# Optimization experiments

Hardware: AMD Instinct MI355X
Metric: run time of the kernel (lower is better)

## Reference

```python
import jax, jax.numpy as jnp
import numpy as np
import math

STRIDES = [4, 8, 16, 32, 64]
SCALES  = [32, 64, 128, 256, 512]
RATIOS  = [2.0, 1.0, 0.5]
GRIDS   = [(200, 304), (100, 152), (50, 76), (25, 38), (13, 19)]  # 800x1216 canvas
LSZ     = [gh * gw * 3 for gh, gw in GRIDS]                        # anchors per level
PRE_NMS_K = [min(1000, n) for n in LSZ]                            # select_by_score (1000, lsz)
IMG_H, IMG_W = 800, 1216
BBOX_CLAMP = math.log(1000.0 / 16.0)
IOU_TH = 0.7
MAX_OUT = 1000
MIN_SIZE = 1e-2
LEVEL_OFFSET = 1e4  # batched-NMS level separation offset


def _make_priors():
    # post.get_priors with loc='corner': anchor centers at stride*i (no +0.5)
    out = []
    for st, (gh, gw), sc in zip(STRIDES, GRIDS, SCALES):
        anc = []
        for r in RATIOS:  # make_anchors_rounded: 1 scale x 3 ratios, rounded
            h = sc * np.sqrt(r)
            w = sc / np.sqrt(r)
            anc.append(np.round(np.array([-w / 2, -h / 2, w / 2, h / 2])))
        anc = np.stack(anc)  # [3,4]
        ys = (np.arange(gh) * st).astype(np.float32)
        xs = (np.arange(gw) * st).astype(np.float32)
        yy, xx = np.meshgrid(ys, xs, indexing='ij')
        shifts = np.stack([xx, yy, xx, yy], axis=-1).reshape(-1, 1, 4)  # [gh*gw,1,4]
        out.append((shifts + anc[None].astype(np.float32)).reshape(-1, 4))
    return np.concatenate(out).astype(np.float32)  # [A,4]


def setup_inputs() -> dict:
    key = jax.random.key(0)
    k1, k2 = jax.random.split(key)
    B, A = 16, sum(LSZ)
    reg = jax.random.normal(k1, (B, A, 4), dtype=jnp.float32) * 0.5  # box deltas
    obj = jax.random.normal(k2, (B, A, 1), dtype=jnp.float32)        # objectness logits
    priors = jnp.asarray(_make_priors())
    return {"reg": reg, "obj": obj, "priors": priors}


def _nms(boxes, init_keep):
    # sequential NMS over score-sorted boxes; boxes already level-offset. [N,4]
    N = boxes.shape[0]
    areas = jnp.clip(boxes[:, 2] - boxes[:, 0], 0) * jnp.clip(boxes[:, 3] - boxes[:, 1], 0)
    rng = jnp.arange(N)

    def body(i, keep):
        b = boxes[i]
        xx1 = jnp.maximum(b[0], boxes[:, 0])
        yy1 = jnp.maximum(b[1], boxes[:, 1])
        xx2 = jnp.minimum(b[2], boxes[:, 2])
        yy2 = jnp.minimum(b[3], boxes[:, 3])
        inter = jnp.clip(xx2 - xx1, 0) * jnp.clip(yy2 - yy1, 0)
        iou = inter / (areas[i] + areas - inter + 1e-9)
        sup = (iou > IOU_TH) & (rng > i) & keep[i]
        return keep & ~sup

    return jax.lax.fori_loop(0, N, body, init_keep)


def reference(reg, obj, priors):
    B = reg.shape[0]
    scores = jax.nn.sigmoid(obj[..., 0])  # [B,A]

    # per-level top-k selection (select_by_score with (1000, lsz))
    off = 0
    idxs, scs, levs = [], [], []
    for l, (n, k) in enumerate(zip(LSZ, PRE_NMS_K)):
        sv, si = jax.lax.top_k(scores[:, off:off + n], k)
        idxs.append(si + off)
        scs.append(sv)
        levs.append(np.full(k, l, np.int32))
        off += n
    idx = jnp.concatenate(idxs, axis=1)       # [B,N] global anchor indices
    sc = jnp.concatenate(scs, axis=1)         # [B,N]
    levels = jnp.asarray(np.concatenate(levs))  # [N]

    reg_s = jnp.take_along_axis(reg, idx[..., None], axis=1)  # [B,N,4]
    pri_s = priors[idx]                                        # [B,N,4]

    # decode_boxes, settings=(1, 1, log(1000/16))
    pw = pri_s[..., 2] - pri_s[..., 0]
    ph = pri_s[..., 3] - pri_s[..., 1]
    pcx = pri_s[..., 0] + 0.5 * pw
    pcy = pri_s[..., 1] + 0.5 * ph
    dx, dy = reg_s[..., 0], reg_s[..., 1]
    dw = jnp.minimum(reg_s[..., 2], BBOX_CLAMP)
    dh = jnp.minimum(reg_s[..., 3], BBOX_CLAMP)
    cx = dx * pw + pcx
    cy = dy * ph + pcy
    w = pw * jnp.exp(dw)
    h = ph * jnp.exp(dh)
    boxes = jnp.stack([cx - 0.5 * w, cy - 0.5 * h, cx + 0.5 * w, cy + 0.5 * h], axis=-1)

    # clamp_to_canvas
    boxes = jnp.stack([
        jnp.clip(boxes[..., 0], 0, IMG_W), jnp.clip(boxes[..., 1], 0, IMG_H),
        jnp.clip(boxes[..., 2], 0, IMG_W), jnp.clip(boxes[..., 3], 0, IMG_H)], axis=-1)

    # remove_small
    small_ok = ((boxes[..., 2] - boxes[..., 0]) > MIN_SIZE) & ((boxes[..., 3] - boxes[..., 1]) > MIN_SIZE)

    # global score-descending order for NMS
    order = jnp.argsort(-sc, axis=1)
    boxes = jnp.take_along_axis(boxes, order[..., None], axis=1)
    sc = jnp.take_along_axis(sc, order, axis=1)
    small_ok = jnp.take_along_axis(small_ok, order, axis=1)
    lev = jnp.take_along_axis(jnp.broadcast_to(levels, sc.shape), order, axis=1)

    # per-level batched NMS via coordinate offset; NMS decisions are non-differentiable
    boxes_off = jax.lax.stop_gradient(boxes) + lev[..., None].astype(boxes.dtype) * LEVEL_OFFSET
    keep = jax.vmap(_nms)(boxes_off, small_ok)  # [B,N] bool

    # take first MAX_OUT kept (already score-sorted), pad with zeros
    rank = jnp.cumsum(keep, axis=1) - 1
    pos = jnp.where(keep & (rank < MAX_OUT), rank, MAX_OUT)  # dump slot MAX_OUT
    out_b = jax.vmap(lambda p, b: jnp.zeros((MAX_OUT + 1, 4), b.dtype).at[p].set(b))(pos, boxes)[:, :MAX_OUT]
    out_s = jax.vmap(lambda p, s: jnp.zeros((MAX_OUT + 1,), s.dtype).at[p].set(s))(pos, sc)[:, :MAX_OUT]
    return jnp.concatenate([out_b, out_s[..., None]], axis=-1)  # [B,1000,5]
```

## Files before the change

### kernel.cpp

```cpp
#include <hip/hip_runtime.h>

typedef unsigned int u32;
typedef unsigned short u16;
typedef unsigned long long u64;

#define NB 16
#define NA 242991
#define NSEL 4741

__device__ __constant__ int c_LN[5]   = {182400, 45600, 11400, 2850, 741};
__device__ __constant__ int c_LOFF[5] = {0, 182400, 228000, 239400, 242250};
__device__ __constant__ int c_LK[5]   = {1000, 1000, 1000, 1000, 741};
__device__ __constant__ int c_SOFF[5] = {0, 1000, 2000, 3000, 4000};
__device__ __constant__ int c_CST[5]  = {0, 64, 80, 84, 85};
__device__ __constant__ int c_CCN[5]  = {64, 16, 4, 1, 1};


__device__ __forceinline__ float xla_tanhf(float x) {
#pragma clang fp contract(off)
  float t = fminf(fmaxf(x, -9.0f), 9.0f);
  float x2 = t * t;
  float p = -2.76076847742355e-16f;
  p = p * x2 + 2.00018790482477e-13f;
  p = p * x2 + -8.60467152213735e-11f;
  p = p * x2 + 5.12229709037114e-08f;
  p = p * x2 + 1.48572235717979e-05f;
  p = p * x2 + 6.37261928875436e-04f;
  p = p * x2 + 4.89352455891786e-03f;
  p = t * p;
  float q = 1.19825839466702e-06f;
  q = q * x2 + 1.18534705686654e-04f;
  q = q * x2 + 2.26843463243900e-03f;
  q = q * x2 + 4.89352518554385e-03f;
  float r = p / q;
  return (fabsf(x) < 0.0004f) ? x : r;
}

__device__ __forceinline__ float ref_sigmoid(float x) {
#pragma clang fp contract(off)
  float t = 0.5f * x;
  float th = xla_tanhf(t);
  return 0.5f + 0.5f * th;
}

__device__ __forceinline__ float xla_expf(float x) {
#pragma clang fp contract(off)
  float fx = x * 1.44269504088896341f + 0.5f;
  fx = floorf(fx);
  float tmp = fx * 0.693359375f;
  float z = fx * -2.12194440e-4f;
  float r = x - tmp;
  r = r - z;
  float r2 = r * r;
  float y = 1.9875691500e-4f;
  y = y * r + 1.3981999507e-3f;
  y = y * r + 8.3334519073e-3f;
  y = y * r + 4.1665795894e-2f;
  y = y * r + 1.6666665459e-1f;
  y = y * r + 5.0000001201e-1f;
  y = y * r2 + r;
  y = y + 1.0f;
  int k = (int)fx;
  float two_k = __uint_as_float((u32)((k + 127) << 23));
  return y * two_k;
}

__device__ __forceinline__ void chunk_map(int c, int& l, int& base, int& n) {
  if (c < 64)      { l = 0; base = c * 2850;                 n = 2850; }
  else if (c < 80) { l = 1; base = 182400 + (c - 64) * 2850; n = 2850; }
  else if (c < 84) { l = 2; base = 228000 + (c - 80) * 2850; n = 2850; }
  else if (c == 84){ l = 3; base = 239400;                   n = 2850; }
  else             { l = 4; base = 242250;                   n = 741;  }
}


__global__ void __launch_bounds__(256) k_hist(const float* __restrict__ obj,
                                              u16* __restrict__ ghist) {
  const int c = blockIdx.x, b = blockIdx.y;
  int l, base, n;
  chunk_map(c, l, base, n);
  __shared__ u32 h[4096];
  for (int i = threadIdx.x; i < 4096; i += 256) h[i] = 0;
  __syncthreads();
  const float* src = obj + (size_t)b * NA + base;
  for (int i = threadIdx.x; i < n; i += 256) {
    float s = ref_sigmoid(src[i]);
    atomicAdd(&h[__float_as_uint(s) >> 18], 1u);
  }
  __syncthreads();
  u32* gh = (u32*)(ghist + ((size_t)b * 86 + c) * 4096);
  for (int i = threadIdx.x; i < 2048; i += 256)
    gh[i] = (h[2 * i] & 0xFFFFu) | (h[2 * i + 1] << 16);
}


__global__ void __launch_bounds__(1024) k_thresh(const u16* __restrict__ ghist,
                                                 int2* __restrict__ binfo,
                                                 u32* __restrict__ ctrs) {
  const int l = blockIdx.x, b = blockIdx.y, t = threadIdx.x;
  const int K = c_LK[l];
  const int bl = b * 5 + l;
  if (t == 0) { ctrs[bl] = 0; ctrs[80 + bl] = 0; }
  __shared__ u32 scan[1024];
  __shared__ int sh_b;
  __shared__ u32 sh_G;
  u32 h0 = 0, h1 = 0, h2 = 0, h3 = 0;
  const int cs = c_CST[l], cn = c_CCN[l];
  const u16* base = ghist + (size_t)b * 86 * 4096 + 4 * t;
  for (int cc = 0; cc < cn; ++cc) {
    uint2 v = *(const uint2*)(base + (size_t)(cs + cc) * 4096);
    h0 += v.x & 0xFFFFu; h1 += v.x >> 16;
    h2 += v.y & 0xFFFFu; h3 += v.y >> 16;
  }
  u32 loc = h0 + h1 + h2 + h3;
  scan[t] = loc;
  __syncthreads();
  for (int d = 1; d < 1024; d <<= 1) {
    u32 v = (t + d < 1024) ? scan[t + d] : 0u;
    __syncthreads();
    scan[t] += v;
    __syncthreads();
  }
  u32 S = scan[t];
  u32 above = S - loc;
  if (S >= (u32)K && above < (u32)K) {
    u32 cacc = above;
    u32 cn2 = cacc + h3;
    if (cn2 >= (u32)K) { sh_b = 4 * t + 3; sh_G = cacc; }
    else {
      cacc = cn2; cn2 = cacc + h2;
      if (cn2 >= (u32)K) { sh_b = 4 * t + 2; sh_G = cacc; }
      else {
        cacc = cn2; cn2 = cacc + h1;
        if (cn2 >= (u32)K) { sh_b = 4 * t + 1; sh_G = cacc; }
        else { cacc = cn2; sh_b = 4 * t; sh_G = cacc; }
      }
    }
  }
  __syncthreads();
  if (t == 0) binfo[bl] = make_int2(sh_b, (int)sh_G);
}


__global__ void __launch_bounds__(256) k_emit(const float* __restrict__ obj,
                                              const int2* __restrict__ binfo,
                                              u64* __restrict__ skey,
                                              u64* __restrict__ candg,
                                              u32* __restrict__ ctrs) {
  const int c = blockIdx.x, b = blockIdx.y;
  int l, base, n;
  chunk_map(c, l, base, n);
  const int bl = b * 5 + l;
  const int bstar = binfo[bl].x;
  const float* src = obj + (size_t)b * NA + base;

  __shared__ u64 bufD[1024];
  __shared__ u64 bufC[2048];
  __shared__ u32 cntDC, gbD, gbC;
  if (threadIdx.x == 0) cntDC = 0;
  __syncthreads();

  const int lane = (int)threadIdx.x & 63;
  const u64 lmask_lt = (lane == 0) ? 0ull : ((~0ull) >> (64 - lane));
  const int iters = (n + 255) >> 8;
  for (int it = 0; it < iters; ++it) {
    int i = it * 256 + (int)threadIdx.x;
    bool valid = i < n;
    float s = ref_sigmoid(valid ? src[i] : 0.0f);
    u32 bits = __float_as_uint(s);
    int bin = (int)(bits >> 18);
    bool isD = valid && (bin > bstar);
    bool isC = valid && (bin == bstar);
    u64 mD = __ballot(isD);
    u64 mC = __ballot(isC);
    u32 bDC = 0;
    if (lane == 0) {
      u32 add = (u32)__popcll(mD) | ((u32)__popcll(mC) << 16);
      if (add) bDC = atomicAdd(&cntDC, add);
    }
    bDC = (u32)__shfl((int)bDC, 0, 64);
    u64 key = ((u64)(bits ^ 0xFFFFFFFFu) << 32) | (u32)(base + i);
    if (isD) {
      u32 p = (bDC & 0xFFFFu) + (u32)__popcll(mD & lmask_lt);
      if (p < 1024) bufD[p] = key;
    }
    if (isC) {
      u32 p = (bDC >> 16) + (u32)__popcll(mC & lmask_lt);
      if (p < 2048) bufC[p] = key;
    }
  }
  __syncthreads();
  const u32 nD = cntDC & 0xFFFFu, nC = cntDC >> 16;
  if (threadIdx.x == 0) {
    gbD = atomicAdd(&ctrs[bl], nD);
    gbC = atomicAdd(&ctrs[80 + bl], nC);
  }
  __syncthreads();
  const u32 gD = gbD, gC = gbC;
  u64* dstD = skey + (size_t)b * NSEL + c_SOFF[l] + gD;
  for (u32 i = threadIdx.x; i < nD; i += 256) dstD[i] = bufD[i];
  u64* dstC = candg + (size_t)bl * 2048;
  for (u32 i = threadIdx.x; i < nC; i += 256) {
    u32 p = gC + i;
    if (p < 2048 && i < 2048) dstC[p] = bufC[i];
  }
}


__device__ __forceinline__ u64 shflx64(u64 v, int d) {
  u32 lo = (u32)v, hi = (u32)(v >> 32);
  lo = (u32)__shfl_xor((int)lo, d, 64);
  hi = (u32)__shfl_xor((int)hi, d, 64);
  return ((u64)hi << 32) | (u64)lo;
}

template <int CTRL>
__device__ __forceinline__ u64 dpp64(u64 v) {
  u32 lo = (u32)__builtin_amdgcn_mov_dpp((int)(u32)v, CTRL, 0xF, 0xF, true);
  u32 hi = (u32)__builtin_amdgcn_mov_dpp((int)(u32)(v >> 32), CTRL, 0xF, 0xF, true);
  return ((u64)hi << 32) | (u64)lo;
}

__global__ void __launch_bounds__(1024) k_selsort(
    const u64* __restrict__ candg, const int2* __restrict__ binfo,
    const u32* __restrict__ ctrs, u64* __restrict__ skey,
    const float* __restrict__ reg, const float* __restrict__ priors,
    float* __restrict__ boxes, float* __restrict__ scoref,
    float* __restrict__ nmsbox, u64* __restrict__ sow) {
  const int l = blockIdx.x, b = blockIdx.y, t = threadIdx.x;
  const int bl = b * 5 + l;
  const int K = c_LK[l];
  const int G = binfo[bl].y;
  u32 cc = ctrs[80 + bl];
  if (cc > 2048) cc = 2048;
  __shared__ u64 sm[4096];
  __shared__ u64 sh_sow[16];
  if (t < 16) sh_sow[t] = 0ull;
  const u64* seg = skey + (size_t)b * NSEL + c_SOFF[l];
  const u64* cnd = candg + (size_t)bl * 2048;

  const int total = G + (int)cc;
  const int NS = (total <= 1024) ? 1024 : (total <= 2048) ? 2048 : 4096;
  const int Q = NS >> 2;
  const bool act = (t < Q);
  const int i0 = 4 * t;

  u64 v0 = ~0ull, v1 = ~0ull, v2 = ~0ull, v3 = ~0ull;
  if (act) {
    auto ld = [&](int i) -> u64 {
      if (i < G) return seg[i];
      int ci = i - G;
      return (ci < (int)cc) ? cnd[ci] : ~0ull;
    };
    v0 = ld(i0); v1 = ld(i0 + 1); v2 = ld(i0 + 2); v3 = ld(i0 + 3);
  }

  auto cs = [](u64& a, u64& b2, bool up) {
    if ((a > b2) == up) { u64 x = a; a = b2; b2 = x; }
  };

  if (act) {
    cs(v0, v1, true);
    cs(v2, v3, false);
    bool up = ((i0 & 4) == 0);
    cs(v0, v2, up); cs(v1, v3, up);
    cs(v0, v1, up); cs(v2, v3, up);
  }
  for (int k = 8; k <= NS; k <<= 1) {
    const bool up = ((i0 & k) == 0);
    for (int j = k >> 1; j >= 256; j >>= 1) {
      if (act) { sm[t] = v0; sm[Q + t] = v1; sm[2 * Q + t] = v2; sm[3 * Q + t] = v3; }
      __syncthreads();
      if (act) {
        const int u = t ^ (j >> 2);
        u64 o0 = sm[u], o1 = sm[Q + u], o2 = sm[2 * Q + u], o3 = sm[3 * Q + u];
        const bool keepmin = (((i0 & j) == 0) == up);
        v0 = keepmin ? (v0 < o0 ? v0 : o0) : (v0 > o0 ? v0 : o0);
        v1 = keepmin ? (v1 < o1 ? v1 : o1) : (v1 > o1 ? v1 : o1);
        v2 = keepmin ? (v2 < o2 ? v2 : o2) : (v2 > o2 ? v2 : o2);
        v3 = keepmin ? (v3 < o3 ? v3 : o3) : (v3 > o3 ? v3 : o3);
      }
      __syncthreads();
    }
    if (act) {
      int jstart = (k >> 1) < 128 ? (k >> 1) : 128;
      for (int j = jstart; j >= 4; j >>= 1) {
        const int d = j >> 2;
        u64 o0, o1, o2, o3;
        if (d == 1) {
          o0 = dpp64<0xB1>(v0); o1 = dpp64<0xB1>(v1);
          o2 = dpp64<0xB1>(v2); o3 = dpp64<0xB1>(v3);
        } else if (d == 2) {
          o0 = dpp64<0x4E>(v0); o1 = dpp64<0x4E>(v1);
          o2 = dpp64<0x4E>(v2); o3 = dpp64<0x4E>(v3);
        } else {
          o0 = shflx64(v0, d); o1 = shflx64(v1, d);
          o2 = shflx64(v2, d); o3 = shflx64(v3, d);
        }
        const bool keepmin = (((t & d) == 0) == up);
        v0 = keepmin ? (v0 < o0 ? v0 : o0) : (v0 > o0 ? v0 : o0);
        v1 = keepmin ? (v1 < o1 ? v1 : o1) : (v1 > o1 ? v1 : o1);
        v2 = keepmin ? (v2 < o2 ? v2 : o2) : (v2 > o2 ? v2 : o2);
        v3 = keepmin ? (v3 < o3 ? v3 : o3) : (v3 > o3 ? v3 : o3);
      }
      cs(v0, v2, up); cs(v1, v3, up);
      cs(v0, v1, up); cs(v2, v3, up);
    }
  }

  __syncthreads();
  if (act) { sm[i0] = v0; sm[i0 + 1] = v1; sm[i0 + 2] = v2; sm[i0 + 3] = v3; }
  __syncthreads();

  u64* dst = skey + (size_t)b * NSEL + c_SOFF[l];

  if (t < K) {
#pragma clang fp contract(off)
    const float lf = (float)l * 10000.0f;
    const int r = t;
    u64 kk = sm[r];
    dst[r] = kk;
    u32 idx = (u32)kk;
    if (idx >= (u32)NA) idx = NA - 1;
    u32 bits = (u32)(kk >> 32) ^ 0xFFFFFFFFu;
    float s = __uint_as_float(bits);
    float4 r4 = ((const float4*)reg)[(size_t)b * NA + idx];
    float4 q4 = ((const float4*)priors)[idx];
    float pw = q4.z - q4.x;
    float ph = q4.w - q4.y;
    float pcx = q4.x + 0.5f * pw;
    float pcy = q4.y + 0.5f * ph;
    float dw = fminf(r4.z, 4.135166556742356f);
    float dh = fminf(r4.w, 4.135166556742356f);
    float cx = r4.x * pw + pcx;
    float cy = r4.y * ph + pcy;
    float w = pw * xla_expf(dw);
    float h = ph * xla_expf(dh);
    float x1 = cx - 0.5f * w;
    float y1 = cy - 0.5f * h;
    float x2 = cx + 0.5f * w;
    float y2 = cy + 0.5f * h;
    x1 = fminf(fmaxf(x1, 0.0f), 1216.0f);
    y1 = fminf(fmaxf(y1, 0.0f), 800.0f);
    x2 = fminf(fmaxf(x2, 0.0f), 1216.0f);
    y2 = fminf(fmaxf(y2, 0.0f), 800.0f);
    bool ok = ((x2 - x1) > 0.01f) && ((y2 - y1) > 0.01f);
    int sidx = c_SOFF[l] + r;
    ((float4*)boxes)[(size_t)b * NSEL + sidx] = make_float4(x1, y1, x2, y2);
    scoref[(size_t)b * NSEL + sidx] = s;
    ((float4*)nmsbox)[(size_t)(b * 5 + l) * 1000 + r] =
        make_float4(x1 + lf, y1 + lf, x2 + lf, y2 + lf);
    if (ok) atomicOr(&sh_sow[r >> 6], 1ull << (r & 63));
  }
  __syncthreads();
  if (t < 16) sow[(size_t)b * 80 + l * 16 + t] = sh_sow[t];
}


__device__ __forceinline__ void tile_map(int k, int& l, int& ti, int& tj) {
  int W;
  if (k < 544) { l = k / 136; k -= l * 136; W = 16; }
  else         { l = 4; k -= 544; W = 12; }
  int a = 0;
  while (k >= W - a) { k -= W - a; a++; }
  ti = a; tj = a + k;
}

__global__ void __launch_bounds__(256) k_nms_build(const float* __restrict__ nmsbox,
                                                   u64* __restrict__ mk) {
#pragma clang fp contract(off)
  const int b = blockIdx.y;
  const int wv = (int)threadIdx.x >> 6;
  const int tid = blockIdx.x * 4 + wv;
  __shared__ float4 cbox[4][64];
  __shared__ float car[4][64];
  if (tid >= 622) return;
  const int lane = (int)threadIdx.x & 63;
  int l, ti, tj;
  tile_map(tid, l, ti, tj);
  const int N = c_LK[l];
  const int bl = b * 5 + l;
  const float4* src = (const float4*)(nmsbox + (size_t)bl * 4000);
  const int i = ti * 64 + lane;
  const int j = tj * 64 + lane;
  const int il = (i < N) ? i : (N - 1);
  const int jl = (j < N) ? j : (N - 1);
  float4 rb = src[il];
  float4 cb0 = src[jl];
  float ra = fmaxf(rb.z - rb.x, 0.0f) * fmaxf(rb.w - rb.y, 0.0f);
  float ca0 = fmaxf(cb0.z - cb0.x, 0.0f) * fmaxf(cb0.w - cb0.y, 0.0f);
  float ra69 = 0.69f * ra;
  cbox[wv][lane] = cb0;
  car[wv][lane] = ca0;
  u32 mlo = 0u, mhi = 0u;
  const double M = 0.7000000178813934326171875;
#pragma unroll
  for (int c = 0; c < 64; ++c) {
    float4 cb = cbox[wv][c];
    float xx1 = fmaxf(rb.x, cb.x);
    float yy1 = fmaxf(rb.y, cb.y);
    float xx2 = fminf(rb.z, cb.z);
    float yy2 = fminf(rb.w, cb.w);
    float inter = fmaxf(xx2 - xx1, 0.0f) * fmaxf(yy2 - yy1, 0.0f);
    if (__any(inter > ra69)) {
      float aj = car[wv][c];
      float den = ((ra + aj) - inter) + 1e-9f;
      bool sup = ((double)inter >= M * (double)den);
      if (c < 32) mlo |= sup ? (1u << c) : 0u;
      else        mhi |= sup ? (1u << (c - 32)) : 0u;
    }
  }
  u64 m = ((u64)mhi << 32) | (u64)mlo;
  if (ti == tj) m &= (lane == 63) ? 0ull : (~0ull << (lane + 1));
  int nc = N - tj * 64;
  if (nc < 64) m &= (1ull << nc) - 1ull;
  if (i < N) mk[(size_t)bl * 16000 + (size_t)tj * 1000 + i] = m;
}


__global__ void __launch_bounds__(1024) k_nms_scan(const u64* __restrict__ mk,
                                                   const u64* __restrict__ sow,
                                                   u64* __restrict__ keepw) {
  const int bl = blockIdx.x;
  const int b = bl / 5, l = bl % 5;
  const int N = c_LK[l];
  const int W = (N + 63) >> 6;
  const int lane = (int)threadIdx.x & 63;
  const int w = (int)threadIdx.x >> 6;
  const bool act = (w < W);
  __shared__ u64 sh_kept[16];

  const u64* rowp = mk + (size_t)bl * 16000 + (size_t)w * 1000;
  u64 acc = act ? ~sow[(size_t)b * 80 + l * 16 + w] : 0ull;

  u64 diag = 0ull;
  if (act) {
    int rd = w * 64 + lane;
    if (rd < N) diag = rowp[rd];
  }
  u64 nxt = (act && w > 0) ? rowp[lane] : 0ull;

  for (int g = 0; g < 16; ++g) {
    if (g >= W) break;
    u64 cur = nxt;
    if (act && w > g + 1) {
      int r = (g + 1) * 64 + lane;
      nxt = (r < N) ? rowp[r] : 0ull;
    } else {
      nxt = 0ull;
    }
    if (w == g) {
      u64 sup = acc;
      u64 pend = __ballot(diag != 0) & ~sup;
      while (pend) {
        int i = __builtin_ctzll(pend);
        u64 rr = __shfl(diag, i, 64);
        sup |= rr;
        pend &= ~sup;
        pend &= ~(1ull << i);
      }
      acc = sup;
      if (lane == 0) sh_kept[g] = ~sup;
    }
    __syncthreads();
    if (act && w > g) {
      u64 K = sh_kept[g];
      u64 c = ((K >> lane) & 1ull) ? cur : 0ull;
#pragma unroll
      for (int d = 1; d < 64; d <<= 1) c |= __shfl_xor(c, d, 64);
      acc |= c;
    }
    __syncthreads();
  }
  if (act && lane == 0) keepw[(size_t)b * 80 + l * 16 + w] = ~acc;
}


__global__ void __launch_bounds__(1024) k_out(const float* __restrict__ boxes,
                                              const float* __restrict__ scoref,
                                              const u64* __restrict__ skey,
                                              const u64* __restrict__ keepw,
                                              float* __restrict__ out) {
  const int l = blockIdx.x, b = blockIdx.y, t = threadIdx.x;
  __shared__ u64 sk[NSEL];
  __shared__ u64 kw[80];
  __shared__ u32 pp[5][17];
  __shared__ u32 sh_T;
  for (int i = t; i < NSEL; i += 1024) sk[i] = skey[(size_t)b * NSEL + i];
  if (t < 80) {
    int l2 = t >> 4, w = t & 15;
    int W = (c_LK[l2] + 63) >> 6;
    kw[t] = (w < W) ? keepw[(size_t)b * 80 + t] : 0ull;
  }
  __syncthreads();
  if (t < 5) {
    u32 acc = 0;
    pp[t][0] = 0;
    for (int w = 0; w < 16; ++w) {
      acc += (u32)__popcll(kw[t * 16 + w]);
      pp[t][w + 1] = acc;
    }
  }
  __syncthreads();
  if (t == 0) sh_T = pp[0][16] + pp[1][16] + pp[2][16] + pp[3][16] + pp[4][16];
  __syncthreads();
  const u32 T = sh_T;
  const int K = c_LK[l];

  for (int r = t; r < K; r += 1024) {
    int s = c_SOFF[l] + r;
    u64 word = kw[l * 16 + (r >> 6)];
    if ((word >> (r & 63)) & 1ull) {
      u32 rank = pp[l][r >> 6] +
                 (u32)__popcll(word & ((r & 63) ? ((1ull << (r & 63)) - 1ull) : 0ull));
      u64 key = sk[s];
#pragma unroll
      for (int l2 = 0; l2 < 5; ++l2) {
        if (l2 == l) continue;
        int lo = 0, hi = c_LK[l2];
        const int base2 = c_SOFF[l2];
        while (lo < hi) {
          int mid = (lo + hi) >> 1;
          if (sk[base2 + mid] < key) lo = mid + 1; else hi = mid;
        }
        u64 w2 = kw[l2 * 16 + (lo >> 6)];
        rank += pp[l2][lo >> 6] +
                (u32)__popcll(w2 & ((lo & 63) ? ((1ull << (lo & 63)) - 1ull) : 0ull));
      }
      if (rank < 1000u) {
        float4 bo = ((const float4*)boxes)[(size_t)b * NSEL + s];
        float* o = out + ((size_t)b * 1000 + rank) * 5;
        o[0] = bo.x; o[1] = bo.y; o[2] = bo.z; o[3] = bo.w;
        o[4] = scoref[(size_t)b * NSEL + s];
      }
    }
  }
  if (l == 0) {
    u32 start = (T < 1000u) ? T : 1000u;
    for (u32 i = start + t; i < 1000u; i += 1024u) {
      float* o = out + ((size_t)b * 1000 + i) * 5;
      o[0] = 0.0f; o[1] = 0.0f; o[2] = 0.0f; o[3] = 0.0f; o[4] = 0.0f;
    }
  }
}


extern "C" void kernel_launch(void* const* d_in, const int* in_sizes, int n_in,
                              void* d_out, int out_size, void* d_ws, size_t ws_size,
                              hipStream_t stream) {
  const float* reg = (const float*)d_in[0];
  const float* obj = (const float*)d_in[1];
  const float* priors = (const float*)d_in[2];
  float* out = (float*)d_out;

  char* ws = (char*)d_ws;
  size_t off = 0;
  auto alloc = [&](size_t bytes) {
    size_t r = off;
    off += (bytes + 255) & ~(size_t)255;
    return r;
  };
  u16* ghist = (u16*)(ws + alloc((size_t)NB * 86 * 4096 * 2));
  u32* ctrs = (u32*)(ws + alloc(160 * 4));
  int2* binfo = (int2*)(ws + alloc(80 * 8));
  u64* candg = (u64*)(ws + alloc((size_t)80 * 2048 * 8));
  u64* skey = (u64*)(ws + alloc((size_t)NB * NSEL * 8));
  float* boxes = (float*)(ws + alloc((size_t)NB * NSEL * 16));
  float* scoref = (float*)(ws + alloc((size_t)NB * NSEL * 4));
  float* nmsbox = (float*)(ws + alloc((size_t)NB * 5 * 1000 * 16));
  u64* sow = (u64*)(ws + alloc((size_t)NB * 80 * 8));
  u64* keepw = (u64*)(ws + alloc((size_t)NB * 80 * 8));
  u64* mk = (u64*)(ws + alloc((size_t)80 * 1000 * 16 * 8));

  k_hist<<<dim3(86, NB), 256, 0, stream>>>(obj, ghist);
  k_thresh<<<dim3(5, NB), 1024, 0, stream>>>(ghist, binfo, ctrs);
  k_emit<<<dim3(86, NB), 256, 0, stream>>>(obj, binfo, skey, candg, ctrs);
  k_selsort<<<dim3(5, NB), 1024, 0, stream>>>(candg, binfo, ctrs, skey, reg,
                                              priors, boxes, scoref, nmsbox, sow);
  k_nms_build<<<dim3(156, NB), 256, 0, stream>>>(nmsbox, mk);
  k_nms_scan<<<dim3(80), 1024, 0, stream>>>(mk, sow, keepw);
  k_out<<<dim3(5, NB), 1024, 0, stream>>>(boxes, scoref, skey, keepw, out);
}
```

Measured before the change: 106.9 us.

## Fuse threshold-bin search into emit kernel and drop k_thresh launch

Removes the separate k_thresh kernel. Each k_emit block now finds the threshold bin itself by scanning the merged per-level histogram from the top bins down in 256-bin chunks, stopping early once it reaches K. Counter zeroing moves into k_hist, and k_selsort takes G from the final counter instead of binfo. This saves a launch and its dependency gap, but every emit block repeats the histogram scan, including the 64 chunk reads per bin for level 0.

```diff
diff --git a/kernel.cpp b/kernel.cpp
--- a/kernel.cpp
+++ b/kernel.cpp
@@ -75,8 +75,13 @@
 
 
 __global__ void __launch_bounds__(256) k_hist(const float* __restrict__ obj,
-                                              u16* __restrict__ ghist) {
+                                              u16* __restrict__ ghist,
+                                              u32* __restrict__ ctrs) {
   const int c = blockIdx.x, b = blockIdx.y;
+  if (c == 0 && threadIdx.x < 5) {
+    ctrs[b * 5 + threadIdx.x] = 0;
+    ctrs[80 + b * 5 + threadIdx.x] = 0;
+  }
   int l, base, n;
   chunk_map(c, l, base, n);
   __shared__ u32 h[4096];
@@ -94,56 +99,8 @@
 }
 
 
-__global__ void __launch_bounds__(1024) k_thresh(const u16* __restrict__ ghist,
-                                                 int2* __restrict__ binfo,
-                                                 u32* __restrict__ ctrs) {
-  const int l = blockIdx.x, b = blockIdx.y, t = threadIdx.x;
-  const int K = c_LK[l];
-  const int bl = b * 5 + l;
-  if (t == 0) { ctrs[bl] = 0; ctrs[80 + bl] = 0; }
-  __shared__ u32 scan[1024];
-  __shared__ int sh_b;
-  __shared__ u32 sh_G;
-  u32 h0 = 0, h1 = 0, h2 = 0, h3 = 0;
-  const int cs = c_CST[l], cn = c_CCN[l];
-  const u16* base = ghist + (size_t)b * 86 * 4096 + 4 * t;
-  for (int cc = 0; cc < cn; ++cc) {
-    uint2 v = *(const uint2*)(base + (size_t)(cs + cc) * 4096);
-    h0 += v.x & 0xFFFFu; h1 += v.x >> 16;
-    h2 += v.y & 0xFFFFu; h3 += v.y >> 16;
-  }
-  u32 loc = h0 + h1 + h2 + h3;
-  scan[t] = loc;
-  __syncthreads();
-  for (int d = 1; d < 1024; d <<= 1) {
-    u32 v = (t + d < 1024) ? scan[t + d] : 0u;
-    __syncthreads();
-    scan[t] += v;
-    __syncthreads();
-  }
-  u32 S = scan[t];
-  u32 above = S - loc;
-  if (S >= (u32)K && above < (u32)K) {
-    u32 cacc = above;
-    u32 cn2 = cacc + h3;
-    if (cn2 >= (u32)K) { sh_b = 4 * t + 3; sh_G = cacc; }
-    else {
-      cacc = cn2; cn2 = cacc + h2;
-      if (cn2 >= (u32)K) { sh_b = 4 * t + 2; sh_G = cacc; }
-      else {
-        cacc = cn2; cn2 = cacc + h1;
-        if (cn2 >= (u32)K) { sh_b = 4 * t + 1; sh_G = cacc; }
-        else { cacc = cn2; sh_b = 4 * t; sh_G = cacc; }
-      }
-    }
-  }
-  __syncthreads();
-  if (t == 0) binfo[bl] = make_int2(sh_b, (int)sh_G);
-}
-
-
 __global__ void __launch_bounds__(256) k_emit(const float* __restrict__ obj,
-                                              const int2* __restrict__ binfo,
+                                              const u16* __restrict__ ghist,
                                               u64* __restrict__ skey,
                                               u64* __restrict__ candg,
                                               u32* __restrict__ ctrs) {
@@ -151,20 +108,53 @@
   int l, base, n;
   chunk_map(c, l, base, n);
   const int bl = b * 5 + l;
-  const int bstar = binfo[bl].x;
+  const int t = (int)threadIdx.x;
+
+  __shared__ u32 ch[256];
+  __shared__ int sh_bstar;
+  const u16* hb = ghist + (size_t)b * 86 * 4096;
+  const int cs2 = c_CST[l], cn2 = c_CCN[l];
+  const int K = c_LK[l];
+  if (t == 0) sh_bstar = -1;
+  __syncthreads();
+  int bstar = 0;
+  u32 acc = 0;
+  for (int cb = 4096 - 256; cb >= 0; cb -= 256) {
+    int bin = cb + t;
+    u32 v = 0;
+    for (int s2 = 0; s2 < cn2; ++s2) v += hb[(size_t)(cs2 + s2) * 4096 + bin];
+    ch[255 - t] = v;
+    __syncthreads();
+    for (int d = 1; d < 256; d <<= 1) {
+      u32 add = (t >= d) ? ch[t - d] : 0u;
+      __syncthreads();
+      ch[t] += add;
+      __syncthreads();
+    }
+    u32 total = ch[255];
+    u32 cum = ch[t];
+    u32 prev = (t == 0) ? 0u : ch[t - 1];
+    if (acc + cum >= (u32)K && acc + prev < (u32)K)
+      sh_bstar = cb + (255 - t);
+    __syncthreads();
+    if (sh_bstar >= 0) { bstar = sh_bstar; break; }
+    acc += total;
+    __syncthreads();
+  }
+  bstar = sh_bstar;
+
   const float* src = obj + (size_t)b * NA + base;
-
   __shared__ u64 bufD[1024];
   __shared__ u64 bufC[2048];
   __shared__ u32 cntDC, gbD, gbC;
-  if (threadIdx.x == 0) cntDC = 0;
-  __syncthreads();
-
-  const int lane = (int)threadIdx.x & 63;
+  if (t == 0) cntDC = 0;
+  __syncthreads();
+
+  const int lane = t & 63;
   const u64 lmask_lt = (lane == 0) ? 0ull : ((~0ull) >> (64 - lane));
   const int iters = (n + 255) >> 8;
   for (int it = 0; it < iters; ++it) {
-    int i = it * 256 + (int)threadIdx.x;
+    int i = it * 256 + t;
     bool valid = i < n;
     float s = ref_sigmoid(valid ? src[i] : 0.0f);
     u32 bits = __float_as_uint(s);
@@ -191,7 +181,7 @@
   }
   __syncthreads();
   const u32 nD = cntDC & 0xFFFFu, nC = cntDC >> 16;
-  if (threadIdx.x == 0) {
+  if (t == 0) {
     gbD = atomicAdd(&ctrs[bl], nD);
     gbC = atomicAdd(&ctrs[80 + bl], nC);
   }
@@ -222,7 +212,7 @@
 }
 
 __global__ void __launch_bounds__(1024) k_selsort(
-    const u64* __restrict__ candg, const int2* __restrict__ binfo,
+    const u64* __restrict__ candg,
     const u32* __restrict__ ctrs, u64* __restrict__ skey,
     const float* __restrict__ reg, const float* __restrict__ priors,
     float* __restrict__ boxes, float* __restrict__ scoref,
@@ -230,7 +220,7 @@
   const int l = blockIdx.x, b = blockIdx.y, t = threadIdx.x;
   const int bl = b * 5 + l;
   const int K = c_LK[l];
-  const int G = binfo[bl].y;
+  const int G = (int)ctrs[bl];
   u32 cc = ctrs[80 + bl];
   if (cc > 2048) cc = 2048;
   __shared__ u64 sm[4096];
@@ -562,7 +552,6 @@
   };
   u16* ghist = (u16*)(ws + alloc((size_t)NB * 86 * 4096 * 2));
   u32* ctrs = (u32*)(ws + alloc(160 * 4));
-  int2* binfo = (int2*)(ws + alloc(80 * 8));
   u64* candg = (u64*)(ws + alloc((size_t)80 * 2048 * 8));
   u64* skey = (u64*)(ws + alloc((size_t)NB * NSEL * 8));
   float* boxes = (float*)(ws + alloc((size_t)NB * NSEL * 16));
@@ -572,10 +561,9 @@
   u64* keepw = (u64*)(ws + alloc((size_t)NB * 80 * 8));
   u64* mk = (u64*)(ws + alloc((size_t)80 * 1000 * 16 * 8));
 
-  k_hist<<<dim3(86, NB), 256, 0, stream>>>(obj, ghist);
-  k_thresh<<<dim3(5, NB), 1024, 0, stream>>>(ghist, binfo, ctrs);
-  k_emit<<<dim3(86, NB), 256, 0, stream>>>(obj, binfo, skey, candg, ctrs);
-  k_selsort<<<dim3(5, NB), 1024, 0, stream>>>(candg, binfo, ctrs, skey, reg,
+  k_hist<<<dim3(86, NB), 256, 0, stream>>>(obj, ghist, ctrs);
+  k_emit<<<dim3(86, NB), 256, 0, stream>>>(obj, ghist, skey, candg, ctrs);
+  k_selsort<<<dim3(5, NB), 1024, 0, stream>>>(candg, ctrs, skey, reg,
                                               priors, boxes, scoref, nmsbox, sow);
   k_nms_build<<<dim3(156, NB), 256, 0, stream>>>(nmsbox, mk);
   k_nms_scan<<<dim3(80), 1024, 0, stream>>>(mk, sow, keepw);
```

After: 101.1 us. 1.06x faster.
